# Kernel tuning notes

Hardware: AMD Instinct MI355X
Metric: run time of the kernel (lower is better)

The kernel has to match this reference:

```python
import jax, jax.numpy as jnp
import numpy as np

N_NODES = 100000
N_EDGES = 1000000
IN_DIM = 64
HID = 64
N_CLUSTER = 30
REG = 0.01


def glorot(key, shape):
    lim = np.sqrt(6.0 / (shape[0] + shape[1]))
    return jax.random.uniform(key, shape, jnp.float32, -lim, lim)


def setup_inputs() -> dict:
    key = jax.random.key(0)
    k1, k2, k3, k4, k5 = jax.random.split(key, 5)
    x = jax.random.normal(k1, (N_NODES, IN_DIM), jnp.float32)
    edge_index = jax.random.randint(k2, (2, N_EDGES), 0, N_NODES, jnp.int64)
    edge_attr = jax.random.uniform(k3, (N_EDGES,), jnp.float32)
    W1 = glorot(k4, (IN_DIM, HID))
    b1 = jnp.zeros((HID,), jnp.float32)
    W2 = glorot(k5, (HID, N_CLUSTER))
    b2 = jnp.zeros((N_CLUSTER,), jnp.float32)
    return {"x": x, "edge_index": edge_index, "edge_attr": edge_attr,
            "W1": W1, "b1": b1, "W2": W2, "b2": b2}


def gcn_conv(x, W, b, src, dst, w):
    # PyG GCNConv with edge weights: add self-loops (weight 1), symmetric norm.
    h = x @ W  # [N, out]
    deg = jax.ops.segment_sum(w, dst, num_segments=N_NODES) + 1.0  # self-loop
    dinv = jax.lax.rsqrt(deg)
    norm = dinv[src] * w * dinv[dst]  # [E]
    agg = jax.ops.segment_sum(norm[:, None] * h[src], dst, num_segments=N_NODES)
    agg = agg + h / deg[:, None]  # self-loop contribution: norm = 1/deg
    return agg + b


def reference(x, edge_index, edge_attr, W1, b1, W2, b2):
    src, dst = edge_index[0], edge_index[1]
    h = jax.nn.relu(gcn_conv(x, W1, b1, src, dst, edge_attr))
    # dropout p=0 -> identity
    X2 = gcn_conv(h, W2, b2, src, dst, edge_attr)
    FX = jax.nn.softmax(X2, axis=-1)  # [N, C]
    FF = jnp.sum(FX[src] * FX[dst], axis=-1)  # [E]
    NFX = jnp.log(1.0 - FX ** 2)  # [N, C]
    preg = -jnp.sum(jnp.log(1.0001 - jnp.exp(jnp.sum(NFX, axis=0))))
    loss = jnp.mean((FF - edge_attr) ** 2)
    return FX, loss + REG * preg
```

## Files before the change

kernel.cpp:

```cpp
#include <hip/hip_runtime.h>
#include <hip/hip_fp16.h>
#include <math.h>

#define N_NODES 100000
#define N_EDGES 1000000
#define IN_DIM 64
#define HID 64
#define NC 30
#define NCP 32
#define REG_C 0.01f

#define NTILES (N_NODES / 16)
#define NBUCK 391
#define EPB_A 2048
#define NBLK_A 489
#define GEMM_BLOCKS 512

typedef _Float16 half8 __attribute__((ext_vector_type(8)));
typedef _Float16 h16x4 __attribute__((ext_vector_type(4)));
typedef float f32x4 __attribute__((ext_vector_type(4)));
typedef float f32x2 __attribute__((ext_vector_type(2)));

__device__ __forceinline__ unsigned char enc_fp8(float v) {
    return (unsigned char)(__builtin_amdgcn_cvt_pk_fp8_f32(v, v, 0, false) & 0xFF);
}
__device__ __forceinline__ float dec_fp8(unsigned char b) {
    return __builtin_amdgcn_cvt_f32_fp8((int)b, 0);
}
__device__ __forceinline__ f32x4 dec_fp8x4(unsigned u) {
    f32x4 r;
    r[0] = __builtin_amdgcn_cvt_f32_fp8((int)u, 0);
    r[1] = __builtin_amdgcn_cvt_f32_fp8((int)u, 1);
    r[2] = __builtin_amdgcn_cvt_f32_fp8((int)u, 2);
    r[3] = __builtin_amdgcn_cvt_f32_fp8((int)u, 3);
    return r;
}
__device__ __forceinline__ float dot4_fp8(unsigned a, unsigned b) {
    float s = __builtin_amdgcn_cvt_f32_fp8((int)a, 0) * __builtin_amdgcn_cvt_f32_fp8((int)b, 0);
    s += __builtin_amdgcn_cvt_f32_fp8((int)a, 1) * __builtin_amdgcn_cvt_f32_fp8((int)b, 1);
    s += __builtin_amdgcn_cvt_f32_fp8((int)a, 2) * __builtin_amdgcn_cvt_f32_fp8((int)b, 2);
    s += __builtin_amdgcn_cvt_f32_fp8((int)a, 3) * __builtin_amdgcn_cvt_f32_fp8((int)b, 3);
    return s;
}

__global__ void hist_gemm(const int* __restrict__ dst, int* __restrict__ histT,
                          const float* __restrict__ X, const float* __restrict__ W,
                          unsigned char* __restrict__ H8) {
    if (blockIdx.x < NBLK_A) {
        __shared__ int cnt[NBUCK];
        for (int i = threadIdx.x; i < NBUCK; i += 256) cnt[i] = 0;
        __syncthreads();
        int e0 = blockIdx.x * EPB_A;
#pragma unroll
        for (int j = 0; j < 8; ++j) {
            int e = e0 + j * 256 + threadIdx.x;
            if (e < N_EDGES) atomicAdd(&cnt[dst[e] >> 8], 1);
        }
        __syncthreads();
        for (int b = threadIdx.x; b < NBUCK; b += 256)
            histT[b * NBLK_A + blockIdx.x] = cnt[b];
        return;
    }
    const int lane = threadIdx.x & 63;
    const int wave = threadIdx.x >> 6;
    const int qd = lane >> 4;
    const int l = lane & 15;
    half8 bfrag[2][4];
#pragma unroll
    for (int kb = 0; kb < 2; ++kb)
#pragma unroll
        for (int t = 0; t < 4; ++t)
#pragma unroll
            for (int j = 0; j < 8; ++j)
                bfrag[kb][t][j] = (_Float16)W[(kb * 32 + qd * 8 + j) * 64 + t * 16 + l];

    const int gb = blockIdx.x - NBLK_A;
    const int waveStride = GEMM_BLOCKS * 4;
    for (int ntile = gb * 4 + wave; ntile < NTILES; ntile += waveStride) {
        const int node0 = ntile * 16;
        const float* arow = X + (size_t)(node0 + l) * 64 + qd * 8;
        half8 af0, af1;
#pragma unroll
        for (int j = 0; j < 8; ++j) {
            af0[j] = (_Float16)arow[j];
            af1[j] = (_Float16)arow[32 + j];
        }
        f32x4 acc[4];
#pragma unroll
        for (int t = 0; t < 4; ++t) acc[t] = (f32x4){0.f, 0.f, 0.f, 0.f};
#pragma unroll
        for (int t = 0; t < 4; ++t) {
            acc[t] = __builtin_amdgcn_mfma_f32_16x16x32_f16(af0, bfrag[0][t], acc[t], 0, 0, 0);
            acc[t] = __builtin_amdgcn_mfma_f32_16x16x32_f16(af1, bfrag[1][t], acc[t], 0, 0, 0);
        }
#pragma unroll
        for (int t = 0; t < 4; ++t)
#pragma unroll
            for (int rr = 0; rr < 4; ++rr)
                H8[(size_t)(node0 + qd * 4 + rr) * 64 + t * 16 + l] = enc_fp8(acc[t][rr]);
    }
}

__global__ void scanA(int* __restrict__ histT, int* __restrict__ bucketTotal) {
    __shared__ int s[NBLK_A];
    int b = blockIdx.x;
    for (int i = threadIdx.x; i < NBLK_A; i += 256) s[i] = histT[b * NBLK_A + i];
    __syncthreads();
    if (threadIdx.x == 0) {
        int run = 0;
        for (int i = 0; i < NBLK_A; ++i) { int t = s[i]; s[i] = run; run += t; }
        bucketTotal[b] = run;
    }
    __syncthreads();
    for (int i = threadIdx.x; i < NBLK_A; i += 256) histT[b * NBLK_A + i] = s[i];
}

__global__ void scanB(const int* __restrict__ bucketTotal, int* __restrict__ bucketBase) {
    __shared__ int s[NBUCK];
    for (int i = threadIdx.x; i < NBUCK; i += 256) s[i] = bucketTotal[i];
    __syncthreads();
    if (threadIdx.x == 0) {
        int run = 0;
        for (int i = 0; i < NBUCK; ++i) { int t = s[i]; s[i] = run; run += t; }
    }
    __syncthreads();
    for (int i = threadIdx.x; i < NBUCK; i += 256) bucketBase[i] = s[i];
    if (threadIdx.x == 0) bucketBase[NBUCK] = N_EDGES;
}

__global__ void scatter_coarse(const int* __restrict__ src, const int* __restrict__ dst,
                               const float* __restrict__ w, const int* __restrict__ histT,
                               const int* __restrict__ bucketBase,
                               int2* __restrict__ sw, unsigned char* __restrict__ dl) {
    __shared__ int cur[NBUCK];
    int bl = blockIdx.x;
    for (int b = threadIdx.x; b < NBUCK; b += 256)
        cur[b] = bucketBase[b] + histT[b * NBLK_A + bl];
    __syncthreads();
    int e0 = bl * EPB_A;
#pragma unroll
    for (int j = 0; j < 8; ++j) {
        int e = e0 + j * 256 + threadIdx.x;
        if (e < N_EDGES) {
            int d = dst[e];
            int pos = atomicAdd(&cur[d >> 8], 1);
            sw[pos] = make_int2(src[e], __float_as_int(w[e]));
            dl[pos] = (unsigned char)(d & 255);
        }
    }
}

__global__ void bucket_deg(const int2* __restrict__ sw, const unsigned char* __restrict__ dl,
                           const int* __restrict__ bucketBase, float* __restrict__ dinv,
                           float* __restrict__ invdeg, int* __restrict__ rowptr) {
    __shared__ int cnt[256];
    __shared__ float degf[256];
    __shared__ int sc[256];
    int b = blockIdx.x, tid = threadIdx.x;
    cnt[tid] = 0; degf[tid] = 0.f;
    __syncthreads();
    int p0 = bucketBase[b], p1 = bucketBase[b + 1];
    for (int p = p0 + tid; p < p1; p += 256) {
        int d = dl[p];
        atomicAdd(&cnt[d], 1);
        atomicAdd(&degf[d], __int_as_float(sw[p].y));
    }
    __syncthreads();
    sc[tid] = cnt[tid];
    __syncthreads();
    for (int off = 1; off < 256; off <<= 1) {
        int t = (tid >= off) ? sc[tid - off] : 0;
        __syncthreads();
        sc[tid] += t;
        __syncthreads();
    }
    int node = b * 256 + tid;
    if (node < N_NODES) {
        float d = degf[tid] + 1.0f;
        dinv[node] = rsqrtf(d);
        invdeg[node] = 1.0f / d;
        rowptr[node] = p0 + sc[tid] - cnt[tid];
    }
    if (b == 0 && tid == 0) rowptr[N_NODES] = N_EDGES;
}

__global__ void bucket_scatter(const int2* __restrict__ sw, const unsigned char* __restrict__ dl,
                               const int* __restrict__ bucketBase, const int* __restrict__ rowptr,
                               const float* __restrict__ dinv,
                               int2* __restrict__ edata2) {
    __shared__ int cur[256];
    __shared__ float ldinv[256];
    int b = blockIdx.x, tid = threadIdx.x;
    int node = b * 256 + tid;
    if (node < N_NODES) { cur[tid] = rowptr[node]; ldinv[tid] = dinv[node]; }
    __syncthreads();
    int p0 = bucketBase[b], p1 = bucketBase[b + 1];
    for (int p = p0 + tid; p < p1; p += 256) {
        int d = dl[p];
        int2 r = sw[p];
        float wv = __int_as_float(r.y);
        float norm = dinv[r.x] * wv * ldinv[d];
        int pos = atomicAdd(&cur[d], 1);
        edata2[pos] = make_int2(r.x, __float_as_int(norm));
    }
}

__global__ void agg64_fused(const int* __restrict__ rowptr, const int2* __restrict__ edata2,
                            const unsigned char* __restrict__ H8, const float* __restrict__ invdeg,
                            const float* __restrict__ b1, _Float16* __restrict__ h2h) {
    const int node = blockIdx.x * 4 + (threadIdx.x >> 6);
    const int lane = threadIdx.x & 63;
    const int s = lane >> 4;
    const int q = lane & 15;
    int p = rowptr[node], end = rowptr[node + 1];
    float acc[4][4] = {};
    for (; p + 15 < end; p += 16) {
        int2 e[4];
#pragma unroll
        for (int g = 0; g < 4; ++g) e[g] = edata2[p + 4 * g + s];
        unsigned u[4];
#pragma unroll
        for (int g = 0; g < 4; ++g)
            u[g] = *(const unsigned*)(H8 + ((unsigned)e[g].x << 6) + (q << 2));
#pragma unroll
        for (int g = 0; g < 4; ++g) {
            float n = __int_as_float(e[g].y);
            f32x4 d = dec_fp8x4(u[g]);
#pragma unroll
            for (int j = 0; j < 4; ++j)
                acc[g][j] += n * d[j];
        }
    }
    {
        int r = end - p;
        int2 e[4];
#pragma unroll
        for (int g = 0; g < 4; ++g) {
            e[g] = make_int2(0, 0);
            if (4 * g + s < r) e[g] = edata2[p + 4 * g + s];
        }
        unsigned u[4];
#pragma unroll
        for (int g = 0; g < 4; ++g)
            u[g] = *(const unsigned*)(H8 + ((unsigned)e[g].x << 6) + (q << 2));
#pragma unroll
        for (int g = 0; g < 4; ++g) {
            float n = __int_as_float(e[g].y);
            f32x4 d = dec_fp8x4(u[g]);
#pragma unroll
            for (int j = 0; j < 4; ++j)
                acc[g][j] += n * d[j];
        }
    }
    float v[4];
#pragma unroll
    for (int j = 0; j < 4; ++j) {
        float t = (acc[0][j] + acc[1][j]) + (acc[2][j] + acc[3][j]);
        t += __shfl_xor(t, 16);
        t += __shfl_xor(t, 32);
        v[j] = t;
    }
    unsigned us = *(const unsigned*)(H8 + ((unsigned)node << 6) + (q << 2));
    float idg = invdeg[node];
    f32x4 bv = *(const f32x4*)(b1 + (q << 2));
    if (s == 0) {
        f32x4 ds = dec_fp8x4(us);
        h16x4 hv;
#pragma unroll
        for (int j = 0; j < 4; ++j) {
            float rj = v[j] + ds[j] * idg + bv[j];
            hv[j] = (_Float16)fmaxf(rj, 0.f);
        }
        *(h16x4*)(h2h + ((unsigned)node << 6) + (q << 2)) = hv;
    }
}

__global__ void linear30(const _Float16* __restrict__ H, const float* __restrict__ W2,
                         __half* __restrict__ HH16) {
    __shared__ float sW[64 * NC];
    __shared__ float sH[8 * 64];
    for (int i = threadIdx.x; i < 64 * NC; i += blockDim.x) sW[i] = W2[i];
    int node0 = blockIdx.x * 8;
    for (int i = threadIdx.x; i < 8 * 64; i += blockDim.x) {
        int n = node0 + (i >> 6);
        sH[i] = (n < N_NODES) ? (float)H[(size_t)n * 64 + (i & 63)] : 0.f;
    }
    __syncthreads();
    int ln = threadIdx.x >> 5;
    int c = threadIdx.x & 31;
    int node = node0 + ln;
    if (node < N_NODES) {
        float acc = 0.f;
        if (c < NC) {
#pragma unroll
            for (int k = 0; k < 64; ++k) acc += sH[ln * 64 + k] * sW[k * NC + c];
        }
        HH16[(size_t)node * NCP + c] = __float2half(acc);
    }
}

__global__ void agg30_softmax_colsum(const int* __restrict__ rowptr, const int2* __restrict__ edata2,
                                     const __half* __restrict__ HH16,
                                     const float* __restrict__ invdeg,
                                     const float* __restrict__ b2, float* __restrict__ FX,
                                     unsigned char* __restrict__ FX8,
                                     float* __restrict__ colsum_part) {
    const int lane = threadIdx.x & 63;
    const int waveInBlock = threadIdx.x >> 6;
    const int n = lane >> 4;
    const int c2 = lane & 15;
    const bool activeC = (c2 < 15);
    const int node = (blockIdx.x * 4 + waveInBlock) * 4 + n;

    float bb0 = activeC ? b2[2 * c2] : 0.f;
    float bb1 = activeC ? b2[2 * c2 + 1] : 0.f;

    int p = rowptr[node], end = rowptr[node + 1];
    float a0[8], a1[8];
#pragma unroll
    for (int k = 0; k < 8; ++k) { a0[k] = 0.f; a1[k] = 0.f; }
    const __half* __restrict__ Hc = HH16 + (c2 << 1);
    for (; p + 7 < end; p += 8) {
        int2 e[8];
#pragma unroll
        for (int k = 0; k < 8; ++k) e[k] = edata2[p + k];
        unsigned h[8];
#pragma unroll
        for (int k = 0; k < 8; ++k)
            h[k] = *(const unsigned*)(Hc + ((unsigned)e[k].x << 5));
#pragma unroll
        for (int k = 0; k < 8; ++k) {
            float nw = __int_as_float(e[k].y);
            float2 hf = __half22float2(*(const __half2*)&h[k]);
            a0[k] += nw * hf.x;
            a1[k] += nw * hf.y;
        }
    }
    {
        int r = end - p;
        int2 e[8];
#pragma unroll
        for (int k = 0; k < 8; ++k) {
            e[k] = make_int2(0, 0);
            if (k < r) e[k] = edata2[p + k];
        }
        unsigned h[8];
#pragma unroll
        for (int k = 0; k < 8; ++k)
            h[k] = *(const unsigned*)(Hc + ((unsigned)e[k].x << 5));
#pragma unroll
        for (int k = 0; k < 8; ++k) {
            float nw = __int_as_float(e[k].y);
            float2 hf = __half22float2(*(const __half2*)&h[k]);
            a0[k] += nw * hf.x;
            a1[k] += nw * hf.y;
        }
    }
    float s0 = ((a0[0] + a0[1]) + (a0[2] + a0[3])) + ((a0[4] + a0[5]) + (a0[6] + a0[7]));
    float s1 = ((a1[0] + a1[1]) + (a1[2] + a1[3])) + ((a1[4] + a1[5]) + (a1[6] + a1[7]));
    unsigned hsu = *(const unsigned*)(Hc + ((unsigned)node << 5));
    float2 hs = __half22float2(*(const __half2*)&hsu);
    float idg = invdeg[node];
    float x0 = activeC ? (s0 + hs.x * idg + bb0) : -INFINITY;
    float x1 = activeC ? (s1 + hs.y * idg + bb1) : -INFINITY;
    float mx = fmaxf(x0, x1);
    mx = fmaxf(mx, __shfl_xor(mx, 1));
    mx = fmaxf(mx, __shfl_xor(mx, 2));
    mx = fmaxf(mx, __shfl_xor(mx, 4));
    mx = fmaxf(mx, __shfl_xor(mx, 8));
    float e0 = activeC ? expf(x0 - mx) : 0.f;
    float e1 = activeC ? expf(x1 - mx) : 0.f;
    float sum = e0 + e1;
    sum += __shfl_xor(sum, 1);
    sum += __shfl_xor(sum, 2);
    sum += __shfl_xor(sum, 4);
    sum += __shfl_xor(sum, 8);
    float fx0 = e0 / sum;
    float fx1 = e1 / sum;

    if (activeC) {
        *(f32x2*)(FX + (size_t)node * NC + 2 * c2) = (f32x2){fx0, fx1};
        unsigned short pk = (unsigned short)((unsigned)enc_fp8(fx0) | ((unsigned)enc_fp8(fx1) << 8));
        *(unsigned short*)(FX8 + ((unsigned)node << 5) + (c2 << 1)) = pk;
    } else {
        *(unsigned short*)(FX8 + ((unsigned)node << 5) + (c2 << 1)) = 0;
    }
    float lacc0 = activeC ? log1pf(-fx0 * fx0) : 0.f;
    float lacc1 = activeC ? log1pf(-fx1 * fx1) : 0.f;
    lacc0 += __shfl_xor(lacc0, 16); lacc0 += __shfl_xor(lacc0, 32);
    lacc1 += __shfl_xor(lacc1, 16); lacc1 += __shfl_xor(lacc1, 32);
    __shared__ float part[4][32];
    if (lane < 16) {
        part[waveInBlock][2 * c2] = lacc0;
        part[waveInBlock][2 * c2 + 1] = lacc1;
    }
    __syncthreads();
    if (threadIdx.x < NC) {
        float v = part[0][threadIdx.x] + part[1][threadIdx.x] +
                  part[2][threadIdx.x] + part[3][threadIdx.x];
        atomicAdd(&colsum_part[(blockIdx.x & 63) * 32 + threadIdx.x], v);
    }
}

__global__ void edge_loss_plain(const int* __restrict__ src, const int* __restrict__ dst,
                                const float* __restrict__ w,
                                const unsigned char* __restrict__ FX8,
                                float* __restrict__ mse_part) {
    int e = blockIdx.x * blockDim.x + threadIdx.x;
    float v = 0.f;
    if (e < N_EDGES) {
        int sn = src[e];
        int dn = dst[e];
        const uint4* rs = (const uint4*)(FX8 + (size_t)sn * NCP);
        const uint4* rd = (const uint4*)(FX8 + (size_t)dn * NCP);
        uint4 a0 = rs[0], a1 = rs[1];
        uint4 b0 = rd[0], b1 = rd[1];
        float ff = dot4_fp8(a0.x, b0.x) + dot4_fp8(a0.y, b0.y) +
                   dot4_fp8(a0.z, b0.z) + dot4_fp8(a0.w, b0.w) +
                   dot4_fp8(a1.x, b1.x) + dot4_fp8(a1.y, b1.y) +
                   dot4_fp8(a1.z, b1.z) + dot4_fp8(a1.w, b1.w);
        float diff = ff - w[e];
        v = diff * diff;
    }
    for (int off = 32; off > 0; off >>= 1) v += __shfl_down(v, off);
    __shared__ float ps[4];
    int lane = threadIdx.x & 63, wv = threadIdx.x >> 6;
    if (lane == 0) ps[wv] = v;
    __syncthreads();
    if (threadIdx.x == 0)
        atomicAdd(&mse_part[blockIdx.x & 63], ps[0] + ps[1] + ps[2] + ps[3]);
}

__global__ void finalize(const float* __restrict__ colsum_part, const float* __restrict__ mse_part,
                         float* __restrict__ out_loss) {
    int t = threadIdx.x;
    float m = mse_part[t];
    for (int off = 32; off > 0; off >>= 1) m += __shfl_down(m, off);
    float term = 0.f;
    if (t < NC) {
        float s = 0.f;
        for (int k = 0; k < 64; ++k) s += colsum_part[k * 32 + t];
        term = logf(1.0001f - expf(s));
    }
    for (int off = 32; off > 0; off >>= 1) term += __shfl_down(term, off);
    if (t == 0)
        out_loss[0] = m / (float)N_EDGES - REG_C * term;
}

extern "C" void kernel_launch(void* const* d_in, const int* in_sizes, int n_in,
                              void* d_out, int out_size, void* d_ws, size_t ws_size,
                              hipStream_t stream) {
    const float* x  = (const float*)d_in[0];
    const int*   ei = (const int*)d_in[1];
    const float* ea = (const float*)d_in[2];
    const float* W1 = (const float*)d_in[3];
    const float* b1 = (const float*)d_in[4];
    const float* W2 = (const float*)d_in[5];
    const float* b2 = (const float*)d_in[6];
    const int* srcI = ei;
    const int* dstI = ei + N_EDGES;

    float* FX   = (float*)d_out;
    float* loss = FX + (size_t)N_NODES * NC;

    float* ws = (float*)d_ws;
    float*         dinv   = ws;
    float*         invdeg = ws + 100000;
    unsigned char* h8     = (unsigned char*)(ws + 200000);
    _Float16*      h2h    = (_Float16*)(ws + 1800000);
    __half*        hh16   = (__half*)(ws + 5000000);
    unsigned char* fx8    = (unsigned char*)(ws + 6600000);
    float*         colsum_part = ws + 7400000;
    float*         mse_part    = ws + 7402048;
    int*           rowptr = (int*)(ws + 7402112);
    int*           histT  = (int*)(ws + 7502114);
    int*           bucketTotal = (int*)(ws + 7693314);
    int*           bucketBase  = (int*)(ws + 7693706);
    int2*          sw     = (int2*)(ws + 7694098);
    unsigned char* dl     = (unsigned char*)(ws + 9694098);
    int2*          edata2 = (int2*)(ws + 9944098);

    hipMemsetAsync(colsum_part, 0, (2048 + 64) * sizeof(float), stream);

    hist_gemm<<<NBLK_A + GEMM_BLOCKS, 256, 0, stream>>>(dstI, histT, x, W1, h8);
    scanA<<<NBUCK, 256, 0, stream>>>(histT, bucketTotal);
    scanB<<<1, 256, 0, stream>>>(bucketTotal, bucketBase);
    scatter_coarse<<<NBLK_A, 256, 0, stream>>>(srcI, dstI, ea, histT, bucketBase, sw, dl);
    bucket_deg<<<NBUCK, 256, 0, stream>>>(sw, dl, bucketBase, dinv, invdeg, rowptr);
    bucket_scatter<<<NBUCK, 256, 0, stream>>>(sw, dl, bucketBase, rowptr, dinv, edata2);
    agg64_fused<<<N_NODES / 4, 256, 0, stream>>>(rowptr, edata2, h8, invdeg, b1, h2h);
    linear30<<<(N_NODES + 7) / 8, 256, 0, stream>>>(h2h, W2, hh16);
    agg30_softmax_colsum<<<N_NODES / 16, 256, 0, stream>>>(rowptr, edata2, hh16, invdeg, b2,
                                                           FX, fx8, colsum_part);
    edge_loss_plain<<<(N_EDGES + 255) / 256, 256, 0, stream>>>(srcI, dstI, ea, fx8, mse_part);
    finalize<<<1, 64, 0, stream>>>(colsum_part, mse_part, loss);
}
```

Before: 282.5 us.

## Replace two-level bucket sort CSR build with global-atomic degree count and direct scatter

New measurement: 364.1 us. 1.29x slower.

```diff
diff --git a/kernel.cpp b/kernel.cpp
--- a/kernel.cpp
+++ b/kernel.cpp
@@ -24,9 +24,6 @@
 __device__ __forceinline__ unsigned char enc_fp8(float v) {
     return (unsigned char)(__builtin_amdgcn_cvt_pk_fp8_f32(v, v, 0, false) & 0xFF);
 }
-__device__ __forceinline__ float dec_fp8(unsigned char b) {
-    return __builtin_amdgcn_cvt_f32_fp8((int)b, 0);
-}
 __device__ __forceinline__ f32x4 dec_fp8x4(unsigned u) {
     f32x4 r;
     r[0] = __builtin_amdgcn_cvt_f32_fp8((int)u, 0);
@@ -43,22 +40,21 @@
     return s;
 }
 
-__global__ void hist_gemm(const int* __restrict__ dst, int* __restrict__ histT,
-                          const float* __restrict__ X, const float* __restrict__ W,
-                          unsigned char* __restrict__ H8) {
+__global__ void deg_gemm(const int* __restrict__ dst, const float* __restrict__ w,
+                         int* __restrict__ cnt, float* __restrict__ degf,
+                         const float* __restrict__ X, const float* __restrict__ W,
+                         unsigned char* __restrict__ H8) {
     if (blockIdx.x < NBLK_A) {
-        __shared__ int cnt[NBUCK];
-        for (int i = threadIdx.x; i < NBUCK; i += 256) cnt[i] = 0;
-        __syncthreads();
         int e0 = blockIdx.x * EPB_A;
 #pragma unroll
         for (int j = 0; j < 8; ++j) {
             int e = e0 + j * 256 + threadIdx.x;
-            if (e < N_EDGES) atomicAdd(&cnt[dst[e] >> 8], 1);
-        }
-        __syncthreads();
-        for (int b = threadIdx.x; b < NBUCK; b += 256)
-            histT[b * NBLK_A + blockIdx.x] = cnt[b];
+            if (e < N_EDGES) {
+                int d = dst[e];
+                atomicAdd(&cnt[d], 1);
+                atomicAdd(&degf[d], w[e]);
+            }
+        }
         return;
     }
     const int lane = threadIdx.x & 63;
@@ -101,72 +97,14 @@
     }
 }
 
-__global__ void scanA(int* __restrict__ histT, int* __restrict__ bucketTotal) {
-    __shared__ int s[NBLK_A];
-    int b = blockIdx.x;
-    for (int i = threadIdx.x; i < NBLK_A; i += 256) s[i] = histT[b * NBLK_A + i];
-    __syncthreads();
-    if (threadIdx.x == 0) {
-        int run = 0;
-        for (int i = 0; i < NBLK_A; ++i) { int t = s[i]; s[i] = run; run += t; }
-        bucketTotal[b] = run;
-    }
-    __syncthreads();
-    for (int i = threadIdx.x; i < NBLK_A; i += 256) histT[b * NBLK_A + i] = s[i];
-}
-
-__global__ void scanB(const int* __restrict__ bucketTotal, int* __restrict__ bucketBase) {
-    __shared__ int s[NBUCK];
-    for (int i = threadIdx.x; i < NBUCK; i += 256) s[i] = bucketTotal[i];
-    __syncthreads();
-    if (threadIdx.x == 0) {
-        int run = 0;
-        for (int i = 0; i < NBUCK; ++i) { int t = s[i]; s[i] = run; run += t; }
-    }
-    __syncthreads();
-    for (int i = threadIdx.x; i < NBUCK; i += 256) bucketBase[i] = s[i];
-    if (threadIdx.x == 0) bucketBase[NBUCK] = N_EDGES;
-}
-
-__global__ void scatter_coarse(const int* __restrict__ src, const int* __restrict__ dst,
-                               const float* __restrict__ w, const int* __restrict__ histT,
-                               const int* __restrict__ bucketBase,
-                               int2* __restrict__ sw, unsigned char* __restrict__ dl) {
-    __shared__ int cur[NBUCK];
-    int bl = blockIdx.x;
-    for (int b = threadIdx.x; b < NBUCK; b += 256)
-        cur[b] = bucketBase[b] + histT[b * NBLK_A + bl];
-    __syncthreads();
-    int e0 = bl * EPB_A;
-#pragma unroll
-    for (int j = 0; j < 8; ++j) {
-        int e = e0 + j * 256 + threadIdx.x;
-        if (e < N_EDGES) {
-            int d = dst[e];
-            int pos = atomicAdd(&cur[d >> 8], 1);
-            sw[pos] = make_int2(src[e], __float_as_int(w[e]));
-            dl[pos] = (unsigned char)(d & 255);
-        }
-    }
-}
-
-__global__ void bucket_deg(const int2* __restrict__ sw, const unsigned char* __restrict__ dl,
-                           const int* __restrict__ bucketBase, float* __restrict__ dinv,
-                           float* __restrict__ invdeg, int* __restrict__ rowptr) {
-    __shared__ int cnt[256];
-    __shared__ float degf[256];
+__global__ void node_scan(const int* __restrict__ cnt, const float* __restrict__ degf,
+                          int* __restrict__ localScan, int* __restrict__ blockTotal,
+                          float* __restrict__ dinv, float* __restrict__ invdeg) {
     __shared__ int sc[256];
     int b = blockIdx.x, tid = threadIdx.x;
-    cnt[tid] = 0; degf[tid] = 0.f;
-    __syncthreads();
-    int p0 = bucketBase[b], p1 = bucketBase[b + 1];
-    for (int p = p0 + tid; p < p1; p += 256) {
-        int d = dl[p];
-        atomicAdd(&cnt[d], 1);
-        atomicAdd(&degf[d], __int_as_float(sw[p].y));
-    }
-    __syncthreads();
-    sc[tid] = cnt[tid];
+    int node = b * 256 + tid;
+    int c = (node < N_NODES) ? cnt[node] : 0;
+    sc[tid] = c;
     __syncthreads();
     for (int off = 1; off < 256; off <<= 1) {
         int t = (tid >= off) ? sc[tid - off] : 0;
@@ -174,34 +112,47 @@
         sc[tid] += t;
         __syncthreads();
     }
-    int node = b * 256 + tid;
     if (node < N_NODES) {
-        float d = degf[tid] + 1.0f;
+        localScan[node] = sc[tid] - c;
+        float d = degf[node] + 1.0f;
         dinv[node] = rsqrtf(d);
         invdeg[node] = 1.0f / d;
-        rowptr[node] = p0 + sc[tid] - cnt[tid];
-    }
-    if (b == 0 && tid == 0) rowptr[N_NODES] = N_EDGES;
-}
-
-__global__ void bucket_scatter(const int2* __restrict__ sw, const unsigned char* __restrict__ dl,
-                               const int* __restrict__ bucketBase, const int* __restrict__ rowptr,
-                               const float* __restrict__ dinv,
-                               int2* __restrict__ edata2) {
-    __shared__ int cur[256];
-    __shared__ float ldinv[256];
-    int b = blockIdx.x, tid = threadIdx.x;
-    int node = b * 256 + tid;
-    if (node < N_NODES) { cur[tid] = rowptr[node]; ldinv[tid] = dinv[node]; }
-    __syncthreads();
-    int p0 = bucketBase[b], p1 = bucketBase[b + 1];
-    for (int p = p0 + tid; p < p1; p += 256) {
-        int d = dl[p];
-        int2 r = sw[p];
-        float wv = __int_as_float(r.y);
-        float norm = dinv[r.x] * wv * ldinv[d];
+    }
+    if (tid == 255) blockTotal[b] = sc[255];
+}
+
+__global__ void scanB(const int* __restrict__ blockTotal, int* __restrict__ tileBase) {
+    __shared__ int s[NBUCK];
+    for (int i = threadIdx.x; i < NBUCK; i += 256) s[i] = blockTotal[i];
+    __syncthreads();
+    if (threadIdx.x == 0) {
+        int run = 0;
+        for (int i = 0; i < NBUCK; ++i) { int t = s[i]; s[i] = run; run += t; }
+    }
+    __syncthreads();
+    for (int i = threadIdx.x; i < NBUCK; i += 256) tileBase[i] = s[i];
+}
+
+__global__ void rowptr_write(const int* __restrict__ localScan, const int* __restrict__ tileBase,
+                             int* __restrict__ rowptr, int* __restrict__ cur) {
+    int node = blockIdx.x * 256 + threadIdx.x;
+    if (node < N_NODES) {
+        int r = tileBase[blockIdx.x] + localScan[node];
+        rowptr[node] = r;
+        cur[node] = r;
+    }
+    if (node == 0) rowptr[N_NODES] = N_EDGES;
+}
+
+__global__ void edge_scatter(const int* __restrict__ src, const int* __restrict__ dst,
+                             const float* __restrict__ w, const float* __restrict__ dinv,
+                             int* __restrict__ cur, int2* __restrict__ edata2) {
+    int e = blockIdx.x * 256 + threadIdx.x;
+    if (e < N_EDGES) {
+        int s = src[e], d = dst[e];
+        float norm = dinv[s] * w[e] * dinv[d];
         int pos = atomicAdd(&cur[d], 1);
-        edata2[pos] = make_int2(r.x, __float_as_int(norm));
+        edata2[pos] = make_int2(s, __float_as_int(norm));
     }
 }
 
@@ -473,21 +424,22 @@
     float*         colsum_part = ws + 7400000;
     float*         mse_part    = ws + 7402048;
     int*           rowptr = (int*)(ws + 7402112);
-    int*           histT  = (int*)(ws + 7502114);
-    int*           bucketTotal = (int*)(ws + 7693314);
-    int*           bucketBase  = (int*)(ws + 7693706);
-    int2*          sw     = (int2*)(ws + 7694098);
-    unsigned char* dl     = (unsigned char*)(ws + 9694098);
-    int2*          edata2 = (int2*)(ws + 9944098);
+    int*           cnt    = (int*)(ws + 7502114);
+    float*         degf   = ws + 7602114;
+    int*           localScan = (int*)(ws + 7702114);
+    int*           blockTotal = (int*)(ws + 7802114);
+    int*           tileBase   = (int*)(ws + 7802505);
+    int*           cur    = (int*)(ws + 7802898);
+    int2*          edata2 = (int2*)(ws + 7902898);
 
     hipMemsetAsync(colsum_part, 0, (2048 + 64) * sizeof(float), stream);
-
-    hist_gemm<<<NBLK_A + GEMM_BLOCKS, 256, 0, stream>>>(dstI, histT, x, W1, h8);
-    scanA<<<NBUCK, 256, 0, stream>>>(histT, bucketTotal);
-    scanB<<<1, 256, 0, stream>>>(bucketTotal, bucketBase);
-    scatter_coarse<<<NBLK_A, 256, 0, stream>>>(srcI, dstI, ea, histT, bucketBase, sw, dl);
-    bucket_deg<<<NBUCK, 256, 0, stream>>>(sw, dl, bucketBase, dinv, invdeg, rowptr);
-    bucket_scatter<<<NBUCK, 256, 0, stream>>>(sw, dl, bucketBase, rowptr, dinv, edata2);
+    hipMemsetAsync(cnt, 0, 200000 * sizeof(float), stream);
+
+    deg_gemm<<<NBLK_A + GEMM_BLOCKS, 256, 0, stream>>>(dstI, ea, cnt, degf, x, W1, h8);
+    node_scan<<<NBUCK, 256, 0, stream>>>(cnt, degf, localScan, blockTotal, dinv, invdeg);
+    scanB<<<1, 256, 0, stream>>>(blockTotal, tileBase);
+    rowptr_write<<<NBUCK, 256, 0, stream>>>(localScan, tileBase, rowptr, cur);
+    edge_scatter<<<(N_EDGES + 255) / 256, 256, 0, stream>>>(srcI, dstI, ea, dinv, cur, edata2);
     agg64_fused<<<N_NODES / 4, 256, 0, stream>>>(rowptr, edata2, h8, invdeg, b1, h2h);
     linear30<<<(N_NODES + 7) / 8, 256, 0, stream>>>(h2h, W2, hh16);
     agg30_softmax_colsum<<<N_NODES / 16, 256, 0, stream>>>(rowptr, edata2, hh16, invdeg, b2,
```

## Fuse degree and scatter kernels, defer source dinv to aggregation, parallelize scans

Applied to the files above, without the earlier changes.

Result: faster. 264.5 us (median of 2 runs) (-6.3%).

```diff
diff --git a/kernel.cpp b/kernel.cpp
--- a/kernel.cpp
+++ b/kernel.cpp
@@ -24,9 +24,6 @@
 __device__ __forceinline__ unsigned char enc_fp8(float v) {
     return (unsigned char)(__builtin_amdgcn_cvt_pk_fp8_f32(v, v, 0, false) & 0xFF);
 }
-__device__ __forceinline__ float dec_fp8(unsigned char b) {
-    return __builtin_amdgcn_cvt_f32_fp8((int)b, 0);
-}
 __device__ __forceinline__ f32x4 dec_fp8x4(unsigned u) {
     f32x4 r;
     r[0] = __builtin_amdgcn_cvt_f32_fp8((int)u, 0);
@@ -102,40 +99,53 @@
 }
 
 __global__ void scanA(int* __restrict__ histT, int* __restrict__ bucketTotal) {
-    __shared__ int s[NBLK_A];
-    int b = blockIdx.x;
-    for (int i = threadIdx.x; i < NBLK_A; i += 256) s[i] = histT[b * NBLK_A + i];
-    __syncthreads();
-    if (threadIdx.x == 0) {
-        int run = 0;
-        for (int i = 0; i < NBLK_A; ++i) { int t = s[i]; s[i] = run; run += t; }
-        bucketTotal[b] = run;
-    }
-    __syncthreads();
-    for (int i = threadIdx.x; i < NBLK_A; i += 256) histT[b * NBLK_A + i] = s[i];
-}
-
-__global__ void scanB(const int* __restrict__ bucketTotal, int* __restrict__ bucketBase) {
-    __shared__ int s[NBUCK];
-    for (int i = threadIdx.x; i < NBUCK; i += 256) s[i] = bucketTotal[i];
-    __syncthreads();
-    if (threadIdx.x == 0) {
-        int run = 0;
-        for (int i = 0; i < NBUCK; ++i) { int t = s[i]; s[i] = run; run += t; }
-    }
-    __syncthreads();
-    for (int i = threadIdx.x; i < NBUCK; i += 256) bucketBase[i] = s[i];
-    if (threadIdx.x == 0) bucketBase[NBUCK] = N_EDGES;
+    __shared__ int sc[256];
+    int b = blockIdx.x, tid = threadIdx.x;
+    int i0 = 2 * tid, i1 = 2 * tid + 1;
+    int v0 = (i0 < NBLK_A) ? histT[b * NBLK_A + i0] : 0;
+    int v1 = (i1 < NBLK_A) ? histT[b * NBLK_A + i1] : 0;
+    int ps = v0 + v1;
+    sc[tid] = ps;
+    __syncthreads();
+    for (int off = 1; off < 256; off <<= 1) {
+        int t = (tid >= off) ? sc[tid - off] : 0;
+        __syncthreads();
+        sc[tid] += t;
+        __syncthreads();
+    }
+    int excl = sc[tid] - ps;
+    if (i0 < NBLK_A) histT[b * NBLK_A + i0] = excl;
+    if (i1 < NBLK_A) histT[b * NBLK_A + i1] = excl + v0;
+    if (tid == 255) bucketTotal[b] = sc[255];
 }
 
 __global__ void scatter_coarse(const int* __restrict__ src, const int* __restrict__ dst,
                                const float* __restrict__ w, const int* __restrict__ histT,
-                               const int* __restrict__ bucketBase,
+                               const int* __restrict__ bucketTotal, int* __restrict__ bucketBase,
                                int2* __restrict__ sw, unsigned char* __restrict__ dl) {
     __shared__ int cur[NBUCK];
-    int bl = blockIdx.x;
-    for (int b = threadIdx.x; b < NBUCK; b += 256)
-        cur[b] = bucketBase[b] + histT[b * NBLK_A + bl];
+    __shared__ int sc[256];
+    int bl = blockIdx.x, tid = threadIdx.x;
+    int i0 = 2 * tid, i1 = 2 * tid + 1;
+    int v0 = (i0 < NBUCK) ? bucketTotal[i0] : 0;
+    int v1 = (i1 < NBUCK) ? bucketTotal[i1] : 0;
+    int ps = v0 + v1;
+    sc[tid] = ps;
+    __syncthreads();
+    for (int off = 1; off < 256; off <<= 1) {
+        int t = (tid >= off) ? sc[tid - off] : 0;
+        __syncthreads();
+        sc[tid] += t;
+        __syncthreads();
+    }
+    int excl = sc[tid] - ps;
+    if (i0 < NBUCK) cur[i0] = excl + histT[i0 * NBLK_A + bl];
+    if (i1 < NBUCK) cur[i1] = excl + v0 + histT[i1 * NBLK_A + bl];
+    if (bl == 0) {
+        if (i0 < NBUCK) bucketBase[i0] = excl;
+        if (i1 < NBUCK) bucketBase[i1] = excl + v0;
+        if (tid == 0) bucketBase[NBUCK] = N_EDGES;
+    }
     __syncthreads();
     int e0 = bl * EPB_A;
 #pragma unroll
@@ -150,12 +160,15 @@
     }
 }
 
-__global__ void bucket_deg(const int2* __restrict__ sw, const unsigned char* __restrict__ dl,
-                           const int* __restrict__ bucketBase, float* __restrict__ dinv,
-                           float* __restrict__ invdeg, int* __restrict__ rowptr) {
+__global__ void fused_bucket(const int2* __restrict__ sw, const unsigned char* __restrict__ dl,
+                             const int* __restrict__ bucketBase, float* __restrict__ dinv,
+                             float* __restrict__ invdeg, int* __restrict__ rowptr,
+                             int2* __restrict__ edata2) {
     __shared__ int cnt[256];
     __shared__ float degf[256];
     __shared__ int sc[256];
+    __shared__ float ldinv[256];
+    __shared__ int cur[256];
     int b = blockIdx.x, tid = threadIdx.x;
     cnt[tid] = 0; degf[tid] = 0.f;
     __syncthreads();
@@ -166,7 +179,8 @@
         atomicAdd(&degf[d], __int_as_float(sw[p].y));
     }
     __syncthreads();
-    sc[tid] = cnt[tid];
+    int c = cnt[tid];
+    sc[tid] = c;
     __syncthreads();
     for (int off = 1; off < 256; off <<= 1) {
         int t = (tid >= off) ? sc[tid - off] : 0;
@@ -175,38 +189,31 @@
         __syncthreads();
     }
     int node = b * 256 + tid;
+    int row = p0 + sc[tid] - c;
+    float dv = 0.f;
     if (node < N_NODES) {
         float d = degf[tid] + 1.0f;
-        dinv[node] = rsqrtf(d);
+        dv = rsqrtf(d);
+        dinv[node] = dv;
         invdeg[node] = 1.0f / d;
-        rowptr[node] = p0 + sc[tid] - cnt[tid];
-    }
-    if (b == 0 && tid == 0) rowptr[N_NODES] = N_EDGES;
-}
-
-__global__ void bucket_scatter(const int2* __restrict__ sw, const unsigned char* __restrict__ dl,
-                               const int* __restrict__ bucketBase, const int* __restrict__ rowptr,
-                               const float* __restrict__ dinv,
-                               int2* __restrict__ edata2) {
-    __shared__ int cur[256];
-    __shared__ float ldinv[256];
-    int b = blockIdx.x, tid = threadIdx.x;
-    int node = b * 256 + tid;
-    if (node < N_NODES) { cur[tid] = rowptr[node]; ldinv[tid] = dinv[node]; }
-    __syncthreads();
-    int p0 = bucketBase[b], p1 = bucketBase[b + 1];
+        rowptr[node] = row;
+    }
+    ldinv[tid] = dv;
+    cur[tid] = row;
+    __syncthreads();
     for (int p = p0 + tid; p < p1; p += 256) {
         int d = dl[p];
         int2 r = sw[p];
-        float wv = __int_as_float(r.y);
-        float norm = dinv[r.x] * wv * ldinv[d];
+        float nw = __int_as_float(r.y) * ldinv[d];
         int pos = atomicAdd(&cur[d], 1);
-        edata2[pos] = make_int2(r.x, __float_as_int(norm));
-    }
+        edata2[pos] = make_int2(r.x, __float_as_int(nw));
+    }
+    if (b == 0 && tid == 0) rowptr[N_NODES] = N_EDGES;
 }
 
 __global__ void agg64_fused(const int* __restrict__ rowptr, const int2* __restrict__ edata2,
-                            const unsigned char* __restrict__ H8, const float* __restrict__ invdeg,
+                            const unsigned char* __restrict__ H8, const float* __restrict__ dinv,
+                            const float* __restrict__ invdeg,
                             const float* __restrict__ b1, _Float16* __restrict__ h2h) {
     const int node = blockIdx.x * 4 + (threadIdx.x >> 6);
     const int lane = threadIdx.x & 63;
@@ -219,12 +226,15 @@
 #pragma unroll
         for (int g = 0; g < 4; ++g) e[g] = edata2[p + 4 * g + s];
         unsigned u[4];
-#pragma unroll
-        for (int g = 0; g < 4; ++g)
+        float dv[4];
+#pragma unroll
+        for (int g = 0; g < 4; ++g) {
             u[g] = *(const unsigned*)(H8 + ((unsigned)e[g].x << 6) + (q << 2));
+            dv[g] = dinv[e[g].x];
+        }
 #pragma unroll
         for (int g = 0; g < 4; ++g) {
-            float n = __int_as_float(e[g].y);
+            float n = dv[g] * __int_as_float(e[g].y);
             f32x4 d = dec_fp8x4(u[g]);
 #pragma unroll
             for (int j = 0; j < 4; ++j)
@@ -240,12 +250,15 @@
             if (4 * g + s < r) e[g] = edata2[p + 4 * g + s];
         }
         unsigned u[4];
-#pragma unroll
-        for (int g = 0; g < 4; ++g)
+        float dv[4];
+#pragma unroll
+        for (int g = 0; g < 4; ++g) {
             u[g] = *(const unsigned*)(H8 + ((unsigned)e[g].x << 6) + (q << 2));
+            dv[g] = dinv[e[g].x];
+        }
 #pragma unroll
         for (int g = 0; g < 4; ++g) {
-            float n = __int_as_float(e[g].y);
+            float n = dv[g] * __int_as_float(e[g].y);
             f32x4 d = dec_fp8x4(u[g]);
 #pragma unroll
             for (int j = 0; j < 4; ++j)
@@ -300,7 +313,7 @@
 }
 
 __global__ void agg30_softmax_colsum(const int* __restrict__ rowptr, const int2* __restrict__ edata2,
-                                     const __half* __restrict__ HH16,
+                                     const __half* __restrict__ HH16, const float* __restrict__ dinv,
                                      const float* __restrict__ invdeg,
                                      const float* __restrict__ b2, float* __restrict__ FX,
                                      unsigned char* __restrict__ FX8,
@@ -325,12 +338,15 @@
 #pragma unroll
         for (int k = 0; k < 8; ++k) e[k] = edata2[p + k];
         unsigned h[8];
-#pragma unroll
-        for (int k = 0; k < 8; ++k)
+        float dv[8];
+#pragma unroll
+        for (int k = 0; k < 8; ++k) {
             h[k] = *(const unsigned*)(Hc + ((unsigned)e[k].x << 5));
+            dv[k] = dinv[e[k].x];
+        }
 #pragma unroll
         for (int k = 0; k < 8; ++k) {
-            float nw = __int_as_float(e[k].y);
+            float nw = dv[k] * __int_as_float(e[k].y);
             float2 hf = __half22float2(*(const __half2*)&h[k]);
             a0[k] += nw * hf.x;
             a1[k] += nw * hf.y;
@@ -345,12 +361,15 @@
             if (k < r) e[k] = edata2[p + k];
         }
         unsigned h[8];
-#pragma unroll
-        for (int k = 0; k < 8; ++k)
+        float dv[8];
+#pragma unroll
+        for (int k = 0; k < 8; ++k) {
             h[k] = *(const unsigned*)(Hc + ((unsigned)e[k].x << 5));
+            dv[k] = dinv[e[k].x];
+        }
 #pragma unroll
         for (int k = 0; k < 8; ++k) {
-            float nw = __int_as_float(e[k].y);
+            float nw = dv[k] * __int_as_float(e[k].y);
             float2 hf = __half22float2(*(const __half2*)&h[k]);
             a0[k] += nw * hf.x;
             a1[k] += nw * hf.y;
@@ -484,14 +503,13 @@
 
     hist_gemm<<<NBLK_A + GEMM_BLOCKS, 256, 0, stream>>>(dstI, histT, x, W1, h8);
     scanA<<<NBUCK, 256, 0, stream>>>(histT, bucketTotal);
-    scanB<<<1, 256, 0, stream>>>(bucketTotal, bucketBase);
-    scatter_coarse<<<NBLK_A, 256, 0, stream>>>(srcI, dstI, ea, histT, bucketBase, sw, dl);
-    bucket_deg<<<NBUCK, 256, 0, stream>>>(sw, dl, bucketBase, dinv, invdeg, rowptr);
-    bucket_scatter<<<NBUCK, 256, 0, stream>>>(sw, dl, bucketBase, rowptr, dinv, edata2);
-    agg64_fused<<<N_NODES / 4, 256, 0, stream>>>(rowptr, edata2, h8, invdeg, b1, h2h);
+    scatter_coarse<<<NBLK_A, 256, 0, stream>>>(srcI, dstI, ea, histT, bucketTotal,
+                                               bucketBase, sw, dl);
+    fused_bucket<<<NBUCK, 256, 0, stream>>>(sw, dl, bucketBase, dinv, invdeg, rowptr, edata2);
+    agg64_fused<<<N_NODES / 4, 256, 0, stream>>>(rowptr, edata2, h8, dinv, invdeg, b1, h2h);
     linear30<<<(N_NODES + 7) / 8, 256, 0, stream>>>(h2h, W2, hh16);
-    agg30_softmax_colsum<<<N_NODES / 16, 256, 0, stream>>>(rowptr, edata2, hh16, invdeg, b2,
-                                                           FX, fx8, colsum_part);
+    agg30_softmax_colsum<<<N_NODES / 16, 256, 0, stream>>>(rowptr, edata2, hh16, dinv, invdeg,
+                                                           b2, FX, fx8, colsum_part);
     edge_loss_plain<<<(N_EDGES + 255) / 256, 256, 0, stream>>>(srcI, dstI, ea, fx8, mse_part);
     finalize<<<1, 64, 0, stream>>>(colsum_part, mse_part, loss);
 }
```
